# Kernel optimization log

Hardware: AMD Instinct MI355X
Metric: run time of the kernel (lower is better)

## Reference

```python
import jax, jax.numpy as jnp
import numpy as np

N_NODES = 50000
N_EDGES = 800000
IN_CH, HID, OUT_CH, N_LAYERS = 512, 64, 40, 64
ALPHA, THETA = 0.5, 1.0


def setup_inputs() -> dict:
    key = jax.random.key(0)
    ks = jax.random.split(key, 6)
    x = jax.random.normal(ks[0], (N_NODES, IN_CH), dtype=jnp.float32)
    edge_index = jax.random.randint(ks[1], (2, N_EDGES), 0, N_NODES, dtype=jnp.int64)
    lin1_w = jax.random.normal(ks[2], (IN_CH, HID), dtype=jnp.float32) * (1.0 / np.sqrt(IN_CH))
    lin1_b = jnp.zeros((HID,), dtype=jnp.float32)
    conv_w = jax.random.normal(ks[3], (N_LAYERS, HID, HID), dtype=jnp.float32) * (1.0 / np.sqrt(HID))
    lin2_w = jax.random.normal(ks[4], (HID, OUT_CH), dtype=jnp.float32) * (1.0 / np.sqrt(HID))
    lin2_b = jnp.zeros((OUT_CH,), dtype=jnp.float32)
    return {"x": x, "edge_index": edge_index, "lin1_w": lin1_w, "lin1_b": lin1_b,
            "conv_w": conv_w, "lin2_w": lin2_w, "lin2_b": lin2_b}


def reference(x, edge_index, lin1_w, lin1_b, conv_w, lin2_w, lin2_b):
    # Eval-mode forward (dropout is identity).
    N = x.shape[0]
    # gcn_norm: add self-loops, symmetric sqrt-degree normalization
    loop = jnp.arange(N, dtype=edge_index.dtype)
    src = jnp.concatenate([edge_index[0], loop])  # [E+N]
    dst = jnp.concatenate([edge_index[1], loop])
    w = jnp.ones(src.shape[0], dtype=x.dtype)
    deg = jax.ops.segment_sum(w, dst, num_segments=N)
    dinv = jnp.where(deg > 0, jax.lax.rsqrt(jnp.maximum(deg, 1e-12)), 0.0)
    norm = (dinv[src] * dinv[dst])[:, None]  # [E+N, 1]

    h = jax.nn.relu(x @ lin1_w + lin1_b)  # [N, HID]
    x0 = h
    L = conv_w.shape[0]
    betas = jnp.log(THETA / jnp.arange(1, L + 1, dtype=x.dtype) + 1.0)

    def step(h, wb):
        W, beta = wb
        # sparse neighbor aggregation: out[i] = sum_{j->i} norm * h[j]
        agg = jax.ops.segment_sum(h[src] * norm, dst, num_segments=N)
        z = (1.0 - ALPHA) * agg + ALPHA * x0            # initial residual
        z = (1.0 - beta) * z + beta * (z @ W)           # identity mapping
        return jax.nn.relu(z), None

    h, _ = jax.lax.scan(step, h, (conv_w, betas))
    out = h @ lin2_w + lin2_b
    return jax.nn.log_softmax(out, axis=1)
```

## Files before the change

kernel.cpp:

```cpp
#include <hip/hip_runtime.h>
#include <hip/hip_bf16.h>
#include <math.h>

#define HID 64


__global__ void count_kernel(const int* __restrict__ dst, int* __restrict__ cnt, int E, int N) {
    int e = blockIdx.x * blockDim.x + threadIdx.x;
    if (e < E) {
        int d = dst[e];
        if ((unsigned)d < (unsigned)N) atomicAdd(&cnt[d], 1);
    }
}

__global__ void dinv_kernel(const int* __restrict__ cnt, float* __restrict__ dinv, int n) {
    int i = blockIdx.x * blockDim.x + threadIdx.x;
    if (i < n) {
        float deg = (float)(cnt[i] + 1);
        dinv[i] = rsqrtf(deg);
    }
}

__global__ __launch_bounds__(1024) void scanA_kernel(const int* __restrict__ cnt,
        int* __restrict__ offs, int* __restrict__ bsum, int n) {
    __shared__ int buf[1024];
    int tid = threadIdx.x;
    int i = blockIdx.x * 1024 + tid;
    int v = (i < n) ? cnt[i] : 0;
    buf[tid] = v;
    __syncthreads();
    for (int off = 1; off < 1024; off <<= 1) {
        int t = (tid >= off) ? buf[tid - off] : 0;
        __syncthreads();
        buf[tid] += t;
        __syncthreads();
    }
    if (i < n) offs[i] = buf[tid] - v;
    if (tid == 1023) bsum[blockIdx.x] = buf[1023];
}

__global__ __launch_bounds__(1024) void scanB_kernel(int* __restrict__ bsum, int nb) {
    __shared__ int buf[1024];
    int tid = threadIdx.x;
    int v = (tid < nb) ? bsum[tid] : 0;
    buf[tid] = v;
    __syncthreads();
    for (int off = 1; off < 1024; off <<= 1) {
        int t = (tid >= off) ? buf[tid - off] : 0;
        __syncthreads();
        buf[tid] += t;
        __syncthreads();
    }
    if (tid < nb) bsum[tid] = buf[tid] - v;
    if (tid == nb - 1) bsum[nb] = buf[tid];
}

__global__ __launch_bounds__(1024) void scanC_kernel(int* __restrict__ offs,
        const int* __restrict__ bsum, int n, int nb) {
    int i = blockIdx.x * 1024 + threadIdx.x;
    if (i < n) offs[i] += bsum[i >> 10];
    if (i == 0) offs[n] = bsum[nb];
}

__global__ void fill_kernel(const int* __restrict__ src, const int* __restrict__ dst,
                            const int* __restrict__ offs, int* __restrict__ cursor,
                            const float* __restrict__ dinv,
                            int2* __restrict__ pack, int E, int N) {
    int e = blockIdx.x * blockDim.x + threadIdx.x;
    if (e < E) {
        int s = src[e], d = dst[e];
        if ((unsigned)s < (unsigned)N && (unsigned)d < (unsigned)N) {
            int pos = atomicAdd(&cursor[d], 1);
            int j = offs[d] + pos;
            if ((unsigned)j < (unsigned)E)
                pack[j] = make_int2(s, __float_as_int(dinv[s] * dinv[d]));
        }
    }
}


__global__ __launch_bounds__(256) void lin1_kernel(const float* __restrict__ x,
        const float* __restrict__ W, const float* __restrict__ b,
        float* __restrict__ out, int n) {
    const int BM = 64, BK = 32;
    __shared__ float As[BM][BK + 1];
    __shared__ float Ws[BK][64];
    int tid = threadIdx.x;
    int row0 = blockIdx.x * BM;
    int tx = tid & 15, ty = tid >> 4;
    float acc[4][4] = {};

    for (int k0 = 0; k0 < 512; k0 += BK) {
        {
            int r = tid >> 3, c4 = tid & 7;
            #pragma unroll
            for (int rr = 0; rr < 2; rr++) {
                int row = row0 + r + rr * 32;
                float4 v = make_float4(0.f, 0.f, 0.f, 0.f);
                if (row < n) v = *(const float4*)&x[(size_t)row * 512 + k0 + c4 * 4];
                As[r + rr * 32][c4 * 4 + 0] = v.x;
                As[r + rr * 32][c4 * 4 + 1] = v.y;
                As[r + rr * 32][c4 * 4 + 2] = v.z;
                As[r + rr * 32][c4 * 4 + 3] = v.w;
            }
        }
        {
            int r = tid >> 4, c4 = tid & 15;
            #pragma unroll
            for (int rr = 0; rr < 2; rr++) {
                float4 v = *(const float4*)&W[(size_t)(k0 + r + rr * 16) * 64 + c4 * 4];
                *(float4*)&Ws[r + rr * 16][c4 * 4] = v;
            }
        }
        __syncthreads();
        #pragma unroll
        for (int kk = 0; kk < BK; kk++) {
            float a0 = As[ty * 4 + 0][kk];
            float a1 = As[ty * 4 + 1][kk];
            float a2 = As[ty * 4 + 2][kk];
            float a3 = As[ty * 4 + 3][kk];
            float4 w = *(float4*)&Ws[kk][tx * 4];
            acc[0][0] += a0 * w.x; acc[0][1] += a0 * w.y; acc[0][2] += a0 * w.z; acc[0][3] += a0 * w.w;
            acc[1][0] += a1 * w.x; acc[1][1] += a1 * w.y; acc[1][2] += a1 * w.z; acc[1][3] += a1 * w.w;
            acc[2][0] += a2 * w.x; acc[2][1] += a2 * w.y; acc[2][2] += a2 * w.z; acc[2][3] += a2 * w.w;
            acc[3][0] += a3 * w.x; acc[3][1] += a3 * w.y; acc[3][2] += a3 * w.z; acc[3][3] += a3 * w.w;
        }
        __syncthreads();
    }
    #pragma unroll
    for (int i = 0; i < 4; i++) {
        int row = row0 + ty * 4 + i;
        if (row < n) {
            #pragma unroll
            for (int j = 0; j < 4; j++) {
                int col = tx * 4 + j;
                float v = acc[i][j] + b[col];
                out[(size_t)row * 64 + col] = fmaxf(v, 0.f);
            }
        }
    }
}


__global__ __launch_bounds__(256) void layer_kernel(
        const float4* __restrict__ h4, const float4* __restrict__ x04,
        float* __restrict__ h_out,
        const int* __restrict__ rowptr, const int2* __restrict__ pack,
        const float* __restrict__ dinv,
        const float* __restrict__ W, float beta, int n) {
    __shared__ float Wsh[HID * HID];
    __shared__ float4 zt[4][HID];
    int tid = threadIdx.x;
    for (int i = tid; i < HID * HID / 4; i += 256)
        ((float4*)Wsh)[i] = ((const float4*)W)[i];
    __syncthreads();
    int lane = tid & 63, wave = tid >> 6;
    int g = lane >> 4;
    int c = lane & 15;
    float omb = 1.0f - beta;

    for (int base = (blockIdx.x * 4 + wave) * 4; base < n; base += gridDim.x * 16) {
        int node = base + g;
        float4 acc = make_float4(0.f, 0.f, 0.f, 0.f);
        if (node < n) {
            float di = dinv[node];
            float d2 = di * di;
            float4 self = h4[(size_t)node * 16 + c];
            acc.x = d2 * self.x; acc.y = d2 * self.y;
            acc.z = d2 * self.z; acc.w = d2 * self.w;
            int e0 = rowptr[node];
            int deg = rowptr[node + 1] - e0;
            int e = 0;
            for (; e + 4 <= deg; e += 4) {
                int2 p0 = pack[e0 + e + 0];
                int2 p1 = pack[e0 + e + 1];
                int2 p2 = pack[e0 + e + 2];
                int2 p3 = pack[e0 + e + 3];
                float4 v0 = h4[(size_t)p0.x * 16 + c];
                float4 v1 = h4[(size_t)p1.x * 16 + c];
                float4 v2 = h4[(size_t)p2.x * 16 + c];
                float4 v3 = h4[(size_t)p3.x * 16 + c];
                float n0 = __int_as_float(p0.y), n1 = __int_as_float(p1.y);
                float n2 = __int_as_float(p2.y), n3 = __int_as_float(p3.y);
                acc.x += n0 * v0.x + n1 * v1.x + n2 * v2.x + n3 * v3.x;
                acc.y += n0 * v0.y + n1 * v1.y + n2 * v2.y + n3 * v3.y;
                acc.z += n0 * v0.z + n1 * v1.z + n2 * v2.z + n3 * v3.z;
                acc.w += n0 * v0.w + n1 * v1.w + n2 * v2.w + n3 * v3.w;
            }
            for (; e < deg; e++) {
                int2 p = pack[e0 + e];
                float4 v = h4[(size_t)p.x * 16 + c];
                float nv = __int_as_float(p.y);
                acc.x += nv * v.x; acc.y += nv * v.y;
                acc.z += nv * v.z; acc.w += nv * v.w;
            }
            float4 x0v = x04[(size_t)node * 16 + c];
            acc.x = 0.5f * acc.x + 0.5f * x0v.x;
            acc.y = 0.5f * acc.y + 0.5f * x0v.y;
            acc.z = 0.5f * acc.z + 0.5f * x0v.z;
            acc.w = 0.5f * acc.w + 0.5f * x0v.w;
        }
        {
            float* zf = (float*)&zt[wave][0];
            zf[(4 * c + 0) * 4 + g] = acc.x;
            zf[(4 * c + 1) * 4 + g] = acc.y;
            zf[(4 * c + 2) * 4 + g] = acc.z;
            zf[(4 * c + 3) * 4 + g] = acc.w;
        }
        float4 mv = make_float4(0.f, 0.f, 0.f, 0.f);
        #pragma unroll 8
        for (int k = 0; k < HID; k++) {
            float4 zk = zt[wave][k];
            float wk = Wsh[k * HID + lane];
            mv.x += zk.x * wk; mv.y += zk.y * wk;
            mv.z += zk.z * wk; mv.w += zk.w * wk;
        }
        float4 zrow = zt[wave][lane];
        float4 y;
        y.x = fmaxf(omb * zrow.x + beta * mv.x, 0.f);
        y.y = fmaxf(omb * zrow.y + beta * mv.y, 0.f);
        y.z = fmaxf(omb * zrow.z + beta * mv.z, 0.f);
        y.w = fmaxf(omb * zrow.w + beta * mv.w, 0.f);
        if (base + 0 < n) h_out[(size_t)(base + 0) * HID + lane] = y.x;
        if (base + 1 < n) h_out[(size_t)(base + 1) * HID + lane] = y.y;
        if (base + 2 < n) h_out[(size_t)(base + 2) * HID + lane] = y.z;
        if (base + 3 < n) h_out[(size_t)(base + 3) * HID + lane] = y.w;
    }
}


__global__ __launch_bounds__(256) void out_kernel(const float* __restrict__ h,
        const float* __restrict__ W2, const float* __restrict__ b2,
        float* __restrict__ out, int n) {
    __shared__ float W2s[64 * 40];
    alignas(16) __shared__ float hs[4][64];
    int tid = threadIdx.x;
    for (int i = tid; i < 64 * 40; i += 256) W2s[i] = W2[i];
    __syncthreads();
    int lane = tid & 63, wave = tid >> 6;
    int c = (lane < 40) ? lane : 0;
    float wc[64];
    #pragma unroll
    for (int k = 0; k < 64; k++) wc[k] = W2s[k * 40 + c];
    float bias = b2[c];
    for (int i = blockIdx.x * 4 + wave; i < n; i += gridDim.x * 4) {
        hs[wave][lane] = h[(size_t)i * 64 + lane];
        float o = bias;
        #pragma unroll
        for (int k4 = 0; k4 < 16; k4++) {
            float4 hb = *(float4*)&hs[wave][k4 * 4];
            o += hb.x * wc[k4 * 4 + 0] + hb.y * wc[k4 * 4 + 1]
               + hb.z * wc[k4 * 4 + 2] + hb.w * wc[k4 * 4 + 3];
        }
        float val = (lane < 40) ? o : -INFINITY;
        float m = val;
        #pragma unroll
        for (int d = 1; d < 64; d <<= 1) m = fmaxf(m, __shfl_xor(m, d, 64));
        float e = (lane < 40) ? expf(o - m) : 0.f;
        float s = e;
        #pragma unroll
        for (int d = 1; d < 64; d <<= 1) s += __shfl_xor(s, d, 64);
        if (lane < 40) out[(size_t)i * 40 + lane] = (o - m) - logf(s);
    }
}

__global__ void zero_out_kernel(float* __restrict__ out, int n) {
    int i = blockIdx.x * blockDim.x + threadIdx.x;
    if (i < n) out[i] = 0.f;
}


extern "C" void kernel_launch(void* const* d_in, const int* in_sizes, int n_in,
                              void* d_out, int out_size, void* d_ws, size_t ws_size,
                              hipStream_t stream) {
    const float* x    = (const float*)d_in[0];
    const int*   ei   = (const int*)d_in[1];
    const float* W1   = (const float*)d_in[2];
    const float* b1   = (const float*)d_in[3];
    const float* Wc   = (const float*)d_in[4];
    const float* W2   = (const float*)d_in[5];
    const float* b2   = (const float*)d_in[6];
    float* outp = (float*)d_out;

    const int N = in_sizes[0] / 512;
    const int E = in_sizes[1] / 2;
    const int L = in_sizes[4] / (HID * HID);

    const int* src = ei;
    const int* dst = ei + E;
    const int NB_SCAN = (N + 1023) / 1024;

    size_t need = ((size_t)N * HID * 3 + (size_t)N * 3 + (N + 1) + (NB_SCAN + 1)) * 4
                + (size_t)E * 8;
    if (ws_size < need) {
        zero_out_kernel<<<(out_size + 255) / 256, 256, 0, stream>>>(outp, out_size);
        return;
    }
    char* p = (char*)d_ws;
    float* hA   = (float*)p;            p += (size_t)N * HID * 4;
    float* hB   = (float*)p;            p += (size_t)N * HID * 4;
    float* x0b  = (float*)p;            p += (size_t)N * HID * 4;
    float* dinv = (float*)p;            p += (size_t)N * 4;
    int2*  pack = (int2*)p;             p += (size_t)E * 8;
    int*   cnt  = (int*)p;              p += (size_t)N * 4;
    int*   offs = (int*)p;              p += (size_t)(N + 1) * 4;
    int*   cursor = (int*)p;            p += (size_t)N * 4;
    int*   bsum = (int*)p;              p += (size_t)(NB_SCAN + 1) * 4;

    hipMemsetAsync(cnt, 0, (size_t)N * 4, stream);
    hipMemsetAsync(cursor, 0, (size_t)N * 4, stream);

    count_kernel<<<(E + 255) / 256, 256, 0, stream>>>(dst, cnt, E, N);
    dinv_kernel<<<(N + 255) / 256, 256, 0, stream>>>(cnt, dinv, N);
    scanA_kernel<<<NB_SCAN, 1024, 0, stream>>>(cnt, offs, bsum, N);
    scanB_kernel<<<1, 1024, 0, stream>>>(bsum, NB_SCAN);
    scanC_kernel<<<NB_SCAN, 1024, 0, stream>>>(offs, bsum, N, NB_SCAN);
    fill_kernel<<<(E + 255) / 256, 256, 0, stream>>>(src, dst, offs, cursor, dinv,
                                                     pack, E, N);

    lin1_kernel<<<(N + 63) / 64, 256, 0, stream>>>(x, W1, b1, x0b, N);

    float* cur_in = x0b;
    float* cur_out = hA;
    for (int l = 0; l < L; l++) {
        float beta = log1pf(1.0f / (float)(l + 1));
        layer_kernel<<<2048, 256, 0, stream>>>((const float4*)cur_in, (const float4*)x0b,
                                               cur_out, offs, pack, dinv,
                                               Wc + (size_t)l * HID * HID, beta, N);
        float* nxt = (cur_out == hA) ? hB : hA;
        cur_in = cur_out;
        cur_out = nxt;
    }

    out_kernel<<<1024, 256, 0, stream>>>(cur_in, W2, b2, outp, N);
}
```

Baseline: 2.549 ms.

## Store layer hidden states in fp16 and prefetch lin1 tiles into registers

Layer activations passed between the 64 propagation layers are now stored as fp16, halving the bytes moved by the random neighbor gathers and the per-layer writes. Accumulation stays in fp32 and x0 is kept in fp32. lin1 also gains register double-buffering of the next K tile to overlap global loads with compute. The cost is reduced precision in the propagated features, with error that can build up over 64 layers.

```diff
diff --git a/kernel.cpp b/kernel.cpp
--- a/kernel.cpp
+++ b/kernel.cpp
@@ -1,8 +1,13 @@
 #include <hip/hip_runtime.h>
 #include <hip/hip_bf16.h>
+#include <hip/hip_fp16.h>
 #include <math.h>
 
 #define HID 64
+
+union HU { __half h; unsigned short u; };
+__device__ inline float h2f(unsigned short u) { HU x; x.u = u; return __half2float(x.h); }
+__device__ inline unsigned short f2h(float f) { HU x; x.h = __float2half(f); return x.u; }
 
 
 __global__ void count_kernel(const int* __restrict__ dst, int* __restrict__ cnt, int E, int N) {
@@ -81,7 +86,7 @@
 
 __global__ __launch_bounds__(256) void lin1_kernel(const float* __restrict__ x,
         const float* __restrict__ W, const float* __restrict__ b,
-        float* __restrict__ out, int n) {
+        float* __restrict__ out32, unsigned short* __restrict__ out16, int n) {
     const int BM = 64, BK = 32;
     __shared__ float As[BM][BK + 1];
     __shared__ float Ws[BK][64];
@@ -90,29 +95,38 @@
     int tx = tid & 15, ty = tid >> 4;
     float acc[4][4] = {};
 
+    int ar = tid >> 3, ac4 = tid & 7;
+    int wr = tid >> 4, wc4 = tid & 15;
+    float4 a_pf[2], w_pf[2];
+
+    #pragma unroll
+    for (int rr = 0; rr < 2; rr++) {
+        int row = row0 + ar + rr * 32;
+        a_pf[rr] = make_float4(0.f, 0.f, 0.f, 0.f);
+        if (row < n) a_pf[rr] = *(const float4*)&x[(size_t)row * 512 + ac4 * 4];
+        w_pf[rr] = *(const float4*)&W[(size_t)(wr + rr * 16) * 64 + wc4 * 4];
+    }
+
     for (int k0 = 0; k0 < 512; k0 += BK) {
-        {
-            int r = tid >> 3, c4 = tid & 7;
+        #pragma unroll
+        for (int rr = 0; rr < 2; rr++) {
+            As[ar + rr * 32][ac4 * 4 + 0] = a_pf[rr].x;
+            As[ar + rr * 32][ac4 * 4 + 1] = a_pf[rr].y;
+            As[ar + rr * 32][ac4 * 4 + 2] = a_pf[rr].z;
+            As[ar + rr * 32][ac4 * 4 + 3] = a_pf[rr].w;
+            *(float4*)&Ws[wr + rr * 16][wc4 * 4] = w_pf[rr];
+        }
+        __syncthreads();
+        int k1 = k0 + BK;
+        if (k1 < 512) {
             #pragma unroll
             for (int rr = 0; rr < 2; rr++) {
-                int row = row0 + r + rr * 32;
-                float4 v = make_float4(0.f, 0.f, 0.f, 0.f);
-                if (row < n) v = *(const float4*)&x[(size_t)row * 512 + k0 + c4 * 4];
-                As[r + rr * 32][c4 * 4 + 0] = v.x;
-                As[r + rr * 32][c4 * 4 + 1] = v.y;
-                As[r + rr * 32][c4 * 4 + 2] = v.z;
-                As[r + rr * 32][c4 * 4 + 3] = v.w;
+                int row = row0 + ar + rr * 32;
+                a_pf[rr] = make_float4(0.f, 0.f, 0.f, 0.f);
+                if (row < n) a_pf[rr] = *(const float4*)&x[(size_t)row * 512 + k1 + ac4 * 4];
+                w_pf[rr] = *(const float4*)&W[(size_t)(k1 + wr + rr * 16) * 64 + wc4 * 4];
             }
         }
-        {
-            int r = tid >> 4, c4 = tid & 15;
-            #pragma unroll
-            for (int rr = 0; rr < 2; rr++) {
-                float4 v = *(const float4*)&W[(size_t)(k0 + r + rr * 16) * 64 + c4 * 4];
-                *(float4*)&Ws[r + rr * 16][c4 * 4] = v;
-            }
-        }
-        __syncthreads();
         #pragma unroll
         for (int kk = 0; kk < BK; kk++) {
             float a0 = As[ty * 4 + 0][kk];
@@ -134,8 +148,9 @@
             #pragma unroll
             for (int j = 0; j < 4; j++) {
                 int col = tx * 4 + j;
-                float v = acc[i][j] + b[col];
-                out[(size_t)row * 64 + col] = fmaxf(v, 0.f);
+                float v = fmaxf(acc[i][j] + b[col], 0.f);
+                out32[(size_t)row * 64 + col] = v;
+                out16[(size_t)row * 64 + col] = f2h(v);
             }
         }
     }
@@ -143,8 +158,8 @@
 
 
 __global__ __launch_bounds__(256) void layer_kernel(
-        const float4* __restrict__ h4, const float4* __restrict__ x04,
-        float* __restrict__ h_out,
+        const ushort4* __restrict__ h16, const float4* __restrict__ x04,
+        unsigned short* __restrict__ h_out,
         const int* __restrict__ rowptr, const int2* __restrict__ pack,
         const float* __restrict__ dinv,
         const float* __restrict__ W, float beta, int n) {
@@ -165,9 +180,9 @@
         if (node < n) {
             float di = dinv[node];
             float d2 = di * di;
-            float4 self = h4[(size_t)node * 16 + c];
-            acc.x = d2 * self.x; acc.y = d2 * self.y;
-            acc.z = d2 * self.z; acc.w = d2 * self.w;
+            ushort4 sv = h16[(size_t)node * 16 + c];
+            acc.x = d2 * h2f(sv.x); acc.y = d2 * h2f(sv.y);
+            acc.z = d2 * h2f(sv.z); acc.w = d2 * h2f(sv.w);
             int e0 = rowptr[node];
             int deg = rowptr[node + 1] - e0;
             int e = 0;
@@ -176,23 +191,23 @@
                 int2 p1 = pack[e0 + e + 1];
                 int2 p2 = pack[e0 + e + 2];
                 int2 p3 = pack[e0 + e + 3];
-                float4 v0 = h4[(size_t)p0.x * 16 + c];
-                float4 v1 = h4[(size_t)p1.x * 16 + c];
-                float4 v2 = h4[(size_t)p2.x * 16 + c];
-                float4 v3 = h4[(size_t)p3.x * 16 + c];
+                ushort4 v0 = h16[(size_t)p0.x * 16 + c];
+                ushort4 v1 = h16[(size_t)p1.x * 16 + c];
+                ushort4 v2 = h16[(size_t)p2.x * 16 + c];
+                ushort4 v3 = h16[(size_t)p3.x * 16 + c];
                 float n0 = __int_as_float(p0.y), n1 = __int_as_float(p1.y);
                 float n2 = __int_as_float(p2.y), n3 = __int_as_float(p3.y);
-                acc.x += n0 * v0.x + n1 * v1.x + n2 * v2.x + n3 * v3.x;
-                acc.y += n0 * v0.y + n1 * v1.y + n2 * v2.y + n3 * v3.y;
-                acc.z += n0 * v0.z + n1 * v1.z + n2 * v2.z + n3 * v3.z;
-                acc.w += n0 * v0.w + n1 * v1.w + n2 * v2.w + n3 * v3.w;
+                acc.x += n0 * h2f(v0.x) + n1 * h2f(v1.x) + n2 * h2f(v2.x) + n3 * h2f(v3.x);
+                acc.y += n0 * h2f(v0.y) + n1 * h2f(v1.y) + n2 * h2f(v2.y) + n3 * h2f(v3.y);
+                acc.z += n0 * h2f(v0.z) + n1 * h2f(v1.z) + n2 * h2f(v2.z) + n3 * h2f(v3.z);
+                acc.w += n0 * h2f(v0.w) + n1 * h2f(v1.w) + n2 * h2f(v2.w) + n3 * h2f(v3.w);
             }
             for (; e < deg; e++) {
                 int2 p = pack[e0 + e];
-                float4 v = h4[(size_t)p.x * 16 + c];
+                ushort4 v = h16[(size_t)p.x * 16 + c];
                 float nv = __int_as_float(p.y);
-                acc.x += nv * v.x; acc.y += nv * v.y;
-                acc.z += nv * v.z; acc.w += nv * v.w;
+                acc.x += nv * h2f(v.x); acc.y += nv * h2f(v.y);
+                acc.z += nv * h2f(v.z); acc.w += nv * h2f(v.w);
             }
             float4 x0v = x04[(size_t)node * 16 + c];
             acc.x = 0.5f * acc.x + 0.5f * x0v.x;
@@ -216,20 +231,15 @@
             mv.z += zk.z * wk; mv.w += zk.w * wk;
         }
         float4 zrow = zt[wave][lane];
-        float4 y;
-        y.x = fmaxf(omb * zrow.x + beta * mv.x, 0.f);
-        y.y = fmaxf(omb * zrow.y + beta * mv.y, 0.f);
-        y.z = fmaxf(omb * zrow.z + beta * mv.z, 0.f);
-        y.w = fmaxf(omb * zrow.w + beta * mv.w, 0.f);
-        if (base + 0 < n) h_out[(size_t)(base + 0) * HID + lane] = y.x;
-        if (base + 1 < n) h_out[(size_t)(base + 1) * HID + lane] = y.y;
-        if (base + 2 < n) h_out[(size_t)(base + 2) * HID + lane] = y.z;
-        if (base + 3 < n) h_out[(size_t)(base + 3) * HID + lane] = y.w;
-    }
-}
-
-
-__global__ __launch_bounds__(256) void out_kernel(const float* __restrict__ h,
+        if (base + 0 < n) h_out[(size_t)(base + 0) * HID + lane] = f2h(fmaxf(omb * zrow.x + beta * mv.x, 0.f));
+        if (base + 1 < n) h_out[(size_t)(base + 1) * HID + lane] = f2h(fmaxf(omb * zrow.y + beta * mv.y, 0.f));
+        if (base + 2 < n) h_out[(size_t)(base + 2) * HID + lane] = f2h(fmaxf(omb * zrow.z + beta * mv.z, 0.f));
+        if (base + 3 < n) h_out[(size_t)(base + 3) * HID + lane] = f2h(fmaxf(omb * zrow.w + beta * mv.w, 0.f));
+    }
+}
+
+
+__global__ __launch_bounds__(256) void out_kernel(const unsigned short* __restrict__ h,
         const float* __restrict__ W2, const float* __restrict__ b2,
         float* __restrict__ out, int n) {
     __shared__ float W2s[64 * 40];
@@ -244,7 +254,7 @@
     for (int k = 0; k < 64; k++) wc[k] = W2s[k * 40 + c];
     float bias = b2[c];
     for (int i = blockIdx.x * 4 + wave; i < n; i += gridDim.x * 4) {
-        hs[wave][lane] = h[(size_t)i * 64 + lane];
+        hs[wave][lane] = h2f(h[(size_t)i * 64 + lane]);
         float o = bias;
         #pragma unroll
         for (int k4 = 0; k4 < 16; k4++) {
@@ -290,22 +300,24 @@
     const int* dst = ei + E;
     const int NB_SCAN = (N + 1023) / 1024;
 
-    size_t need = ((size_t)N * HID * 3 + (size_t)N * 3 + (N + 1) + (NB_SCAN + 1)) * 4
+    size_t need = (size_t)N * HID * 4
+                + (size_t)N * HID * 2 * 2
+                + ((size_t)N * 3 + (N + 1) + (NB_SCAN + 1)) * 4
                 + (size_t)E * 8;
     if (ws_size < need) {
         zero_out_kernel<<<(out_size + 255) / 256, 256, 0, stream>>>(outp, out_size);
         return;
     }
     char* p = (char*)d_ws;
-    float* hA   = (float*)p;            p += (size_t)N * HID * 4;
-    float* hB   = (float*)p;            p += (size_t)N * HID * 4;
-    float* x0b  = (float*)p;            p += (size_t)N * HID * 4;
-    float* dinv = (float*)p;            p += (size_t)N * 4;
-    int2*  pack = (int2*)p;             p += (size_t)E * 8;
-    int*   cnt  = (int*)p;              p += (size_t)N * 4;
-    int*   offs = (int*)p;              p += (size_t)(N + 1) * 4;
-    int*   cursor = (int*)p;            p += (size_t)N * 4;
-    int*   bsum = (int*)p;              p += (size_t)(NB_SCAN + 1) * 4;
+    float* x0b  = (float*)p;               p += (size_t)N * HID * 4;
+    unsigned short* hA16 = (unsigned short*)p;  p += (size_t)N * HID * 2;
+    unsigned short* hB16 = (unsigned short*)p;  p += (size_t)N * HID * 2;
+    float* dinv = (float*)p;               p += (size_t)N * 4;
+    int2*  pack = (int2*)p;                p += (size_t)E * 8;
+    int*   cnt  = (int*)p;                 p += (size_t)N * 4;
+    int*   offs = (int*)p;                 p += (size_t)(N + 1) * 4;
+    int*   cursor = (int*)p;               p += (size_t)N * 4;
+    int*   bsum = (int*)p;                 p += (size_t)(NB_SCAN + 1) * 4;
 
     hipMemsetAsync(cnt, 0, (size_t)N * 4, stream);
     hipMemsetAsync(cursor, 0, (size_t)N * 4, stream);
@@ -318,16 +330,16 @@
     fill_kernel<<<(E + 255) / 256, 256, 0, stream>>>(src, dst, offs, cursor, dinv,
                                                      pack, E, N);
 
-    lin1_kernel<<<(N + 63) / 64, 256, 0, stream>>>(x, W1, b1, x0b, N);
-
-    float* cur_in = x0b;
-    float* cur_out = hA;
+    lin1_kernel<<<(N + 63) / 64, 256, 0, stream>>>(x, W1, b1, x0b, hA16, N);
+
+    unsigned short* cur_in = hA16;
+    unsigned short* cur_out = hB16;
     for (int l = 0; l < L; l++) {
         float beta = log1pf(1.0f / (float)(l + 1));
-        layer_kernel<<<2048, 256, 0, stream>>>((const float4*)cur_in, (const float4*)x0b,
+        layer_kernel<<<2048, 256, 0, stream>>>((const ushort4*)cur_in, (const float4*)x0b,
                                                cur_out, offs, pack, dinv,
                                                Wc + (size_t)l * HID * HID, beta, N);
-        float* nxt = (cur_out == hA) ? hB : hA;
+        unsigned short* nxt = cur_in;
         cur_in = cur_out;
         cur_out = nxt;
     }
```

Result: faster. 2.198 ms (-13.8%).
